# Performance work log

Hardware: AMD Instinct MI355X
Metric: run time of the kernel (lower is better)

The kernel has to match this reference:

```python
import jax, jax.numpy as jnp
import numpy as np

HIDDEN = 2048
HEADS = 16
HEAD_DIM = HIDDEN // HEADS
ROPE_BASE = 10000.0
BSZ, SEQ = 1, 2048
F32_MIN = jnp.finfo(jnp.float32).min


def setup_inputs() -> dict:
    key = jax.random.key(0)
    ks = jax.random.split(key, 5)
    hidden_states = jax.random.normal(ks[0], (BSZ, SEQ, HIDDEN), dtype=jnp.float32)
    # causal additive mask: 0 on/below diagonal, large negative above
    causal = jnp.tril(jnp.ones((SEQ, SEQ), dtype=bool))
    attention_mask = jnp.where(causal, 0.0, F32_MIN)[None, None, :, :].astype(jnp.float32)
    position_ids = jnp.broadcast_to(jnp.arange(SEQ, dtype=jnp.int32)[None, :], (BSZ, SEQ))
    scale = 1.0 / np.sqrt(HIDDEN)
    Wq = jax.random.normal(ks[1], (HIDDEN, HIDDEN), dtype=jnp.float32) * scale
    Wk = jax.random.normal(ks[2], (HIDDEN, HIDDEN), dtype=jnp.float32) * scale
    Wv = jax.random.normal(ks[3], (HIDDEN, HIDDEN), dtype=jnp.float32) * scale
    Wo = jax.random.normal(ks[4], (HIDDEN, HIDDEN), dtype=jnp.float32) * scale
    return {"hidden_states": hidden_states, "attention_mask": attention_mask,
            "position_ids": position_ids, "Wq": Wq, "Wk": Wk, "Wv": Wv, "Wo": Wo}


def _rotate_half(x):
    x1, x2 = jnp.split(x, 2, axis=-1)
    return jnp.concatenate([-x2, x1], axis=-1)


def _rope_cos_sin(position_ids, dtype):
    # [b, s] int -> cos/sin [b, 1, s, head_dim]
    inv_freq = 1.0 / (ROPE_BASE ** (jnp.arange(0, HEAD_DIM, 2, dtype=jnp.float32) / HEAD_DIM))
    freqs = position_ids.astype(jnp.float32)[..., None] * inv_freq  # [b, s, d/2]
    emb = jnp.concatenate([freqs, freqs], axis=-1)  # [b, s, d]
    return jnp.cos(emb)[:, None].astype(dtype), jnp.sin(emb)[:, None].astype(dtype)


def reference(hidden_states, attention_mask, position_ids, Wq, Wk, Wv, Wo):
    b, s, _ = hidden_states.shape

    def proj(W):  # [b, s, hidden] -> [b, h, s, d]
        return jnp.einsum('bsm,mn->bsn', hidden_states, W).reshape(b, s, HEADS, HEAD_DIM).transpose(0, 2, 1, 3)

    q, k, v = proj(Wq), proj(Wk), proj(Wv)
    cos, sin = _rope_cos_sin(position_ids, q.dtype)
    q = q * cos + _rotate_half(q) * sin
    k = k * cos + _rotate_half(k) * sin

    scores = jnp.einsum('bhqd,bhkd->bhqk', q, k) / np.sqrt(HEAD_DIM)
    scores = jnp.maximum(scores + attention_mask, F32_MIN)
    attn = jax.nn.softmax(scores.astype(jnp.float32), axis=-1).astype(q.dtype)
    out = jnp.einsum('bhqk,bhkd->bhqd', attn, v)  # [b, h, s, d]
    out = out.transpose(0, 2, 1, 3).reshape(b, s, HIDDEN)
    return jnp.einsum('bsm,mn->bsn', out, Wo)
```

## Files before the change

kernel.cpp:

```cpp
#include <hip/hip_runtime.h>
#include <hip/hip_bf16.h>
#include <math.h>

#define SEQn 2048
#define HID  2048
#define NH   16
#define HD   128

typedef __attribute__((ext_vector_type(8))) __bf16 bf16x8;
typedef __attribute__((ext_vector_type(4))) float  f32x4;

#define MFMA16(a,b,c) __builtin_amdgcn_mfma_f32_16x16x32_bf16((a),(b),(c),0,0,0)

__device__ __forceinline__ ushort f2bf(float f) {
  union { float f; unsigned u; } v; v.f = f;
  unsigned r = v.u + 0x7fffu + ((v.u >> 16) & 1u);
  return (ushort)(r >> 16);
}
__device__ __forceinline__ float bf2f(ushort u) {
  union { unsigned u; float f; } v; v.u = ((unsigned)u) << 16; return v.f;
}
__device__ __forceinline__ void split2(float x, ushort& h, ushort& l) {
  h = f2bf(x);
  l = f2bf(x - bf2f(h));
}
__device__ __forceinline__ void gl_lds16(const ushort* g, ushort* l) {
  __builtin_amdgcn_global_load_lds((const __attribute__((address_space(1))) unsigned int*)g,
                                   (__attribute__((address_space(3))) unsigned int*)l, 16, 0, 0);
}

__global__ void k_rope_tables(const int* __restrict__ pos,
                              float* __restrict__ cosT, float* __restrict__ sinT) {
  int t = threadIdx.x;
  int s = blockIdx.x * 4 + (t >> 6), i = t & 63;
  float p = (float)pos[s];
  float ex = (float)(2 * i) / 128.0f;
  float invf = 1.0f / powf(10000.0f, ex);
  float f = p * invf;
  cosT[s * 64 + i] = cosf(f);
  sinT[s * 64 + i] = sinf(f);
}

__global__ void k_split(const float* __restrict__ x,
                        ushort* __restrict__ hi, ushort* __restrict__ lo, int n4) {
  int i = blockIdx.x * blockDim.x + threadIdx.x;
  if (i >= n4) return;
  const float4 v = ((const float4*)x)[i];
  ushort4 h, l;
  split2(v.x, h.x, l.x); split2(v.y, h.y, l.y);
  split2(v.z, h.z, l.z); split2(v.w, h.w, l.w);
  ((ushort4*)hi)[i] = h; ((ushort4*)lo)[i] = l;
}

__global__ void k_splitT3(const float* __restrict__ W0, const float* __restrict__ W1,
                          const float* __restrict__ W2,
                          ushort* __restrict__ Th, ushort* __restrict__ Tl) {
  __shared__ float tile[32][33];
  const float* W = (blockIdx.z == 0) ? W0 : (blockIdx.z == 1) ? W1 : W2;
  ushort* Thz = Th + (size_t)blockIdx.z * HID * HID;
  ushort* Tlz = Tl + (size_t)blockIdx.z * HID * HID;
  int kb = blockIdx.x * 32, nb = blockIdx.y * 32;
  int tx = threadIdx.x, ty = threadIdx.y;
#pragma unroll
  for (int r = 0; r < 4; r++)
    tile[ty + r * 8][tx] = W[(size_t)(kb + ty + r * 8) * HID + nb + tx];
  __syncthreads();
#pragma unroll
  for (int r = 0; r < 4; r++) {
    int n = nb + ty + r * 8, k = kb + tx;
    ushort h, l; split2(tile[tx][ty + r * 8], h, l);
    Thz[(size_t)n * HID + k] = h;
    Tlz[(size_t)n * HID + k] = l;
  }
}

template<int DB>
__global__ __launch_bounds__(512) void k_gemm_x3(
    const ushort* __restrict__ Ah, const ushort* __restrict__ Al,
    const ushort* __restrict__ Bh, const ushort* __restrict__ Bl,
    float* __restrict__ C) {
  __shared__ alignas(16) ushort lds[DB][4][4096];
  const int t = threadIdx.x, lane = t & 63, w = t >> 6;
  const int bm = blockIdx.y * 128, bn = blockIdx.x * 128;
  const size_t zb = (size_t)blockIdx.z * HID * HID;
  const int lr = lane & 15, lg = lane >> 4;
  const int sr = t >> 2, sc = (t & 3) * 8;
  const ushort* ga  = Ah + (size_t)(bm + sr) * HID + sc;
  const ushort* gal = Al + (size_t)(bm + sr) * HID + sc;
  const ushort* gb  = Bh + zb + (size_t)(bn + sr) * HID + sc;
  const ushort* gbl = Bl + zb + (size_t)(bn + sr) * HID + sc;
  const int wr = (w & 3) * 32, wc = (w >> 2) * 64;
  f32x4 acc[2][4] = {};
  int cur = 0;
  if constexpr (DB == 2) {
    gl_lds16(ga,  &lds[0][0][w * 512]);
    gl_lds16(gal, &lds[0][1][w * 512]);
    gl_lds16(gb,  &lds[0][2][w * 512]);
    gl_lds16(gbl, &lds[0][3][w * 512]);
  }
  for (int k0 = 0; k0 < HID; k0 += 32) {
    __syncthreads();
    if constexpr (DB == 2) {
      if (k0 + 32 < HID) {
        gl_lds16(ga  + k0 + 32, &lds[cur ^ 1][0][w * 512]);
        gl_lds16(gal + k0 + 32, &lds[cur ^ 1][1][w * 512]);
        gl_lds16(gb  + k0 + 32, &lds[cur ^ 1][2][w * 512]);
        gl_lds16(gbl + k0 + 32, &lds[cur ^ 1][3][w * 512]);
      }
    } else {
      gl_lds16(ga  + k0, &lds[0][0][w * 512]);
      gl_lds16(gal + k0, &lds[0][1][w * 512]);
      gl_lds16(gb  + k0, &lds[0][2][w * 512]);
      gl_lds16(gbl + k0, &lds[0][3][w * 512]);
      __syncthreads();
    }
    bf16x8 a_h[2], a_l[2], b_h[4], b_l[4];
#pragma unroll
    for (int mi = 0; mi < 2; mi++) {
      int ro = (wr + mi * 16 + lr) * 32 + lg * 8;
      a_h[mi] = *(const bf16x8*)&lds[cur][0][ro];
      a_l[mi] = *(const bf16x8*)&lds[cur][1][ro];
    }
#pragma unroll
    for (int ni = 0; ni < 4; ni++) {
      int ro = (wc + ni * 16 + lr) * 32 + lg * 8;
      b_h[ni] = *(const bf16x8*)&lds[cur][2][ro];
      b_l[ni] = *(const bf16x8*)&lds[cur][3][ro];
    }
#pragma unroll
    for (int mi = 0; mi < 2; mi++)
#pragma unroll
      for (int ni = 0; ni < 4; ni++) {
        acc[mi][ni] = MFMA16(a_h[mi], b_h[ni], acc[mi][ni]);
        acc[mi][ni] = MFMA16(a_h[mi], b_l[ni], acc[mi][ni]);
        acc[mi][ni] = MFMA16(a_l[mi], b_h[ni], acc[mi][ni]);
      }
    if constexpr (DB == 2) cur ^= 1;
  }
  float* Cz = C + (size_t)blockIdx.z * SEQn * HID;
#pragma unroll
  for (int mi = 0; mi < 2; mi++)
#pragma unroll
    for (int ni = 0; ni < 4; ni++)
#pragma unroll
      for (int j = 0; j < 4; j++) {
        int row = bm + wr + mi * 16 + lg * 4 + j;
        int col = bn + wc + ni * 16 + lr;
        Cz[(size_t)row * HID + col] = acc[mi][ni][j];
      }
}

__global__ void k_rope_qk(const float* __restrict__ Qf, const float* __restrict__ Kf,
                          const float* __restrict__ cosT, const float* __restrict__ sinT,
                          ushort* __restrict__ Qhh, ushort* __restrict__ Qll,
                          ushort* __restrict__ Khh, ushort* __restrict__ Kll) {
  int t = threadIdx.x;
  int s = blockIdx.x * 4 + (t >> 6), h = blockIdx.y, d = t & 63;
  const float scale = 0.08838834764831845f;
  float c = cosT[s * 64 + d], sn = sinT[s * 64 + d];
  size_t in0  = (size_t)s * HID + h * HD + d;
  size_t out0 = ((size_t)h * SEQn + s) * HD + d;
  ushort hh, ll;
  {
    float q1 = Qf[in0] * scale, q2 = Qf[in0 + 64] * scale;
    split2(q1 * c - q2 * sn, hh, ll); Qhh[out0] = hh;      Qll[out0] = ll;
    split2(q2 * c + q1 * sn, hh, ll); Qhh[out0 + 64] = hh; Qll[out0 + 64] = ll;
  }
  {
    float k1 = Kf[in0], k2 = Kf[in0 + 64];
    split2(k1 * c - k2 * sn, hh, ll); Khh[out0] = hh;      Kll[out0] = ll;
    split2(k2 * c + k1 * sn, hh, ll); Khh[out0 + 64] = hh; Kll[out0 + 64] = ll;
  }
}

__global__ void k_transpose_v(const float* __restrict__ Vf,
                              ushort* __restrict__ Vth, ushort* __restrict__ Vtl) {
  __shared__ float tile[32][33];
  int h = blockIdx.x, db = blockIdx.y * 32, sb = blockIdx.z * 32;
  int tx = threadIdx.x, ty = threadIdx.y;
#pragma unroll
  for (int r = 0; r < 4; r++)
    tile[ty + r * 8][tx] = Vf[(size_t)(sb + ty + r * 8) * HID + h * HD + db + tx];
  __syncthreads();
#pragma unroll
  for (int r = 0; r < 4; r++) {
    int d = db + ty + r * 8, s = sb + tx;
    ushort hh, ll; split2(tile[tx][ty + r * 8], hh, ll);
    size_t o = ((size_t)h * HD + d) * SEQn + s;
    Vth[o] = hh; Vtl[o] = ll;
  }
}

__global__ __launch_bounds__(256) void k_attn(
    const ushort* __restrict__ Qhh, const ushort* __restrict__ Qll,
    const ushort* __restrict__ Khh, const ushort* __restrict__ Kll,
    const ushort* __restrict__ Vth, const ushort* __restrict__ Vtl,
    ushort* __restrict__ Ohi, ushort* __restrict__ Olo) {
  __shared__ alignas(16) ushort sKh[2][8192];
  __shared__ alignas(16) ushort sKl[2][8192];
  __shared__ alignas(16) ushort sVh[2][8192];
  __shared__ alignas(16) ushort sVl[2][8192];
  __shared__ alignas(16) ushort sP[4][1152];
  const int t = threadIdx.x, lane = t & 63, w = t >> 6;
  const int flat = blockIdx.y * 32 + blockIdx.x;
  const int s_ = flat & 255, halfsel = flat >> 8;
  const int qt_ = s_ & 31, h_ = s_ >> 5;
  const int qt = halfsel ? (31 - qt_) : qt_;
  const int h  = halfsel ? (8 + h_) : h_;
  const int qb = qt * 64;
  const int lr = lane & 15, lg = lane >> 4;
  const int q0 = qb + w * 16;
  const size_t qoff = ((size_t)h * SEQn + q0 + lr) * HD + lg * 8;
  bf16x8 qh[4], ql[4];
#pragma unroll
  for (int ks = 0; ks < 4; ks++) {
    qh[ks] = *(const bf16x8*)(Qhh + qoff + ks * 32);
    ql[ks] = *(const bf16x8*)(Qll + qoff + ks * 32);
  }
  const int cc = (w << 6) | lane;
  const int rK = cc >> 4;
  const int cbK = (((cc & 15) << 4) ^ ((rK & 7) << 4)) >> 1;
  const size_t srcKo = (size_t)(h * SEQn + rK) * HD + cbK;
  const int rV = cc >> 3;
  const int cbV = (((cc & 7) << 4) ^ ((rV & 7) << 4)) >> 1;
  const size_t srcVo = (size_t)(h * HD + rV) * SEQn + cbV;

  f32x4 o[8] = {};
  float mrow[4], lrow[4];
#pragma unroll
  for (int j = 0; j < 4; j++) { mrow[j] = -INFINITY; lrow[j] = 0.f; }
  ushort* myp = &sP[w][0];

  {
    const ushort* gKh = Khh + srcKo;
    const ushort* gKl = Kll + srcKo;
    const ushort* gVh = Vth + srcVo;
    const ushort* gVl = Vtl + srcVo;
#pragma unroll
    for (int i = 0; i < 4; i++) {
      gl_lds16(gKh + (size_t)i * 16 * HD,   &sKh[0][(w + i * 4) * 512]);
      gl_lds16(gKl + (size_t)i * 16 * HD,   &sKl[0][(w + i * 4) * 512]);
      gl_lds16(gVh + (size_t)i * 32 * SEQn, &sVh[0][(w + i * 4) * 512]);
      gl_lds16(gVl + (size_t)i * 32 * SEQn, &sVl[0][(w + i * 4) * 512]);
    }
  }

  for (int kv0 = 0; kv0 <= qb; kv0 += 64) {
    const int cur = (kv0 >> 6) & 1;
    __syncthreads();
    if (kv0 + 64 <= qb) {
      const ushort* gKh = Khh + srcKo + (size_t)(kv0 + 64) * HD;
      const ushort* gKl = Kll + srcKo + (size_t)(kv0 + 64) * HD;
      const ushort* gVh = Vth + srcVo + kv0 + 64;
      const ushort* gVl = Vtl + srcVo + kv0 + 64;
#pragma unroll
      for (int i = 0; i < 4; i++) {
        gl_lds16(gKh + (size_t)i * 16 * HD,   &sKh[cur ^ 1][(w + i * 4) * 512]);
        gl_lds16(gKl + (size_t)i * 16 * HD,   &sKl[cur ^ 1][(w + i * 4) * 512]);
        gl_lds16(gVh + (size_t)i * 32 * SEQn, &sVh[cur ^ 1][(w + i * 4) * 512]);
        gl_lds16(gVl + (size_t)i * 32 * SEQn, &sVl[cur ^ 1][(w + i * 4) * 512]);
      }
    }
    f32x4 s4[4] = {};
    __builtin_amdgcn_s_setprio(1);
#pragma unroll
    for (int ni = 0; ni < 4; ni++) {
      const int kr = ni * 16 + lr;
      const int kbase = kr * 128;
      const int ksw = (kr & 7) << 4;
#pragma unroll
      for (int ks = 0; ks < 4; ks++) {
        const int off = kbase + (((ks * 64 + lg * 16) ^ ksw) >> 1);
        bf16x8 kh = *(const bf16x8*)&sKh[cur][off];
        bf16x8 kl = *(const bf16x8*)&sKl[cur][off];
        s4[ni] = MFMA16(qh[ks], kh, s4[ni]);
        s4[ni] = MFMA16(qh[ks], kl, s4[ni]);
        s4[ni] = MFMA16(ql[ks], kh, s4[ni]);
      }
    }
    __builtin_amdgcn_s_setprio(0);
    float sf[4];
    ushort pl[4][4];
#pragma unroll
    for (int j = 0; j < 4; j++) {
      const int row = q0 + lg * 4 + j;
      float sc[4];
#pragma unroll
      for (int ni = 0; ni < 4; ni++) {
        int col = kv0 + ni * 16 + lr;
        sc[ni] = (col <= row) ? s4[ni][j] : -INFINITY;
      }
      float rm = fmaxf(fmaxf(sc[0], sc[1]), fmaxf(sc[2], sc[3]));
#pragma unroll
      for (int off = 1; off < 16; off <<= 1) rm = fmaxf(rm, __shfl_xor(rm, off));
      float mn = fmaxf(mrow[j], rm);
      sf[j] = __expf(mrow[j] - mn);
      float rs = 0.f;
#pragma unroll
      for (int ni = 0; ni < 4; ni++) {
        float pv = __expf(sc[ni] - mn);
        rs += pv;
        ushort hh, ll; split2(pv, hh, ll);
        myp[(lg * 4 + j) * 72 + ni * 16 + lr] = hh;
        pl[j][ni] = ll;
      }
#pragma unroll
      for (int off = 1; off < 16; off <<= 1) rs += __shfl_xor(rs, off);
      lrow[j] = lrow[j] * sf[j] + rs;
      mrow[j] = mn;
    }
#pragma unroll
    for (int nn = 0; nn < 8; nn++) {
      o[nn][0] *= sf[0]; o[nn][1] *= sf[1]; o[nn][2] *= sf[2]; o[nn][3] *= sf[3];
    }
    bf16x8 p0h = *(const bf16x8*)&myp[lr * 72 + lg * 8];
    bf16x8 p1h = *(const bf16x8*)&myp[lr * 72 + lg * 8 + 32];
#pragma unroll
    for (int j = 0; j < 4; j++)
#pragma unroll
      for (int ni = 0; ni < 4; ni++)
        myp[(lg * 4 + j) * 72 + ni * 16 + lr] = pl[j][ni];
    bf16x8 p0l = *(const bf16x8*)&myp[lr * 72 + lg * 8];
    bf16x8 p1l = *(const bf16x8*)&myp[lr * 72 + lg * 8 + 32];
    __builtin_amdgcn_s_setprio(1);
#pragma unroll
    for (int nn = 0; nn < 8; nn++) {
      const int d = nn * 16 + lr;
      const int vbase = d * 64;
      const int vsw = (d & 7) << 4;
      const int o0 = vbase + (((lg * 16) ^ vsw) >> 1);
      const int o1 = vbase + (((lg * 16 + 64) ^ vsw) >> 1);
      bf16x8 vh0 = *(const bf16x8*)&sVh[cur][o0];
      bf16x8 vl0 = *(const bf16x8*)&sVl[cur][o0];
      bf16x8 vh1 = *(const bf16x8*)&sVh[cur][o1];
      bf16x8 vl1 = *(const bf16x8*)&sVl[cur][o1];
      o[nn] = MFMA16(p0h, vh0, o[nn]);
      o[nn] = MFMA16(p0h, vl0, o[nn]);
      o[nn] = MFMA16(p0l, vh0, o[nn]);
      o[nn] = MFMA16(p1h, vh1, o[nn]);
      o[nn] = MFMA16(p1h, vl1, o[nn]);
      o[nn] = MFMA16(p1l, vh1, o[nn]);
    }
    __builtin_amdgcn_s_setprio(0);
  }
#pragma unroll
  for (int nn = 0; nn < 8; nn++)
#pragma unroll
    for (int j = 0; j < 4; j++) {
      int row = q0 + lg * 4 + j;
      int col = h * HD + nn * 16 + lr;
      ushort hh, ll; split2(o[nn][j] / lrow[j], hh, ll);
      Ohi[(size_t)row * HID + col] = hh;
      Olo[(size_t)row * HID + col] = ll;
    }
}

extern "C" void kernel_launch(void* const* d_in, const int* in_sizes, int n_in,
                              void* d_out, int out_size, void* d_ws, size_t ws_size,
                              hipStream_t stream) {
  const float* Hf  = (const float*)d_in[0];
  const int*   pos = (const int*)d_in[2];
  const float* Wq  = (const float*)d_in[3];
  const float* Wk  = (const float*)d_in[4];
  const float* Wv  = (const float*)d_in[5];
  const float* Wo  = (const float*)d_in[6];

  char* ws = (char*)d_ws;
  const size_t SZ_TBL = (size_t)SEQn * 64 * 4;
  const size_t SZ_BF  = (size_t)SEQn * HID * 2;
  const size_t SZ_F   = (size_t)SEQn * HID * 4;
  const size_t PLANE  = (size_t)HID * HID;
  size_t off = 0;
  float*  cosT = (float*)(ws + off);  off += SZ_TBL;
  float*  sinT = (float*)(ws + off);  off += SZ_TBL;
  ushort* Hhi  = (ushort*)(ws + off); off += SZ_BF;
  ushort* Hlo  = (ushort*)(ws + off); off += SZ_BF;
  ushort* W3h  = (ushort*)(ws + off); off += 3 * SZ_BF;
  ushort* W3l  = (ushort*)(ws + off); off += 3 * SZ_BF;
  float*  QKVf = (float*)(ws + off);  off += 3 * SZ_F;
  float*  Qf = QKVf;
  float*  Kf = QKVf + (size_t)SEQn * HID;
  float*  Vf = QKVf + 2 * (size_t)SEQn * HID;
  ushort* Qhh = W3h;
  ushort* Qll = W3h + PLANE;
  ushort* Khh = W3h + 2 * PLANE;
  ushort* Kll = W3l;
  ushort* Vth = W3l + PLANE;
  ushort* Vtl = W3l + 2 * PLANE;
  ushort* Ohi = (ushort*)Kf;
  ushort* Olo = (ushort*)((char*)Kf + SZ_BF);

  const int n4 = SEQn * HID / 4;

  k_rope_tables<<<dim3(SEQn / 4), dim3(256), 0, stream>>>(pos, cosT, sinT);
  k_split<<<dim3(n4 / 256), dim3(256), 0, stream>>>(Hf, Hhi, Hlo, n4);

  k_splitT3<<<dim3(64, 64, 3), dim3(32, 8), 0, stream>>>(Wq, Wk, Wv, W3h, W3l);

  k_gemm_x3<1><<<dim3(16, 16, 3), dim3(512), 0, stream>>>(Hhi, Hlo, W3h, W3l, QKVf);

  k_rope_qk<<<dim3(SEQn / 4, NH), dim3(256), 0, stream>>>(Qf, Kf, cosT, sinT, Qhh, Qll, Khh, Kll);
  k_transpose_v<<<dim3(NH, 4, 64), dim3(32, 8), 0, stream>>>(Vf, Vth, Vtl);

  k_attn<<<dim3(SEQn / 64, NH), dim3(256), 0, stream>>>(Qhh, Qll, Khh, Kll, Vth, Vtl, Ohi, Olo);

  k_splitT3<<<dim3(64, 64, 1), dim3(32, 8), 0, stream>>>(Wo, Wo, Wo, W3h, W3l);
  k_gemm_x3<2><<<dim3(16, 16, 1), dim3(512), 0, stream>>>(Ohi, Olo, W3h, W3l, (float*)d_out);
}
```

Baseline: 585.7 us.

## Drop K/V double buffering and read V directly from global memory

Removes the double-buffered LDS staging for K and V. K is now loaded into a single LDS buffer each iteration, with an extra barrier before use, and the V fragments are read straight from global memory inside the PV loop. This cuts LDS usage from about 137KB to about 41KB, which may allow more resident blocks per CU. In exchange the K load is no longer overlapped with compute, and V is read from global memory by each wave with no sharing through LDS.

```diff
diff --git a/kernel.cpp b/kernel.cpp
--- a/kernel.cpp
+++ b/kernel.cpp
@@ -196,10 +196,8 @@
     const ushort* __restrict__ Khh, const ushort* __restrict__ Kll,
     const ushort* __restrict__ Vth, const ushort* __restrict__ Vtl,
     ushort* __restrict__ Ohi, ushort* __restrict__ Olo) {
-  __shared__ alignas(16) ushort sKh[2][8192];
-  __shared__ alignas(16) ushort sKl[2][8192];
-  __shared__ alignas(16) ushort sVh[2][8192];
-  __shared__ alignas(16) ushort sVl[2][8192];
+  __shared__ alignas(16) ushort sKh[8192];
+  __shared__ alignas(16) ushort sKl[8192];
   __shared__ alignas(16) ushort sP[4][1152];
   const int t = threadIdx.x, lane = t & 63, w = t >> 6;
   const int flat = blockIdx.y * 32 + blockIdx.x;
@@ -221,9 +219,6 @@
   const int rK = cc >> 4;
   const int cbK = (((cc & 15) << 4) ^ ((rK & 7) << 4)) >> 1;
   const size_t srcKo = (size_t)(h * SEQn + rK) * HD + cbK;
-  const int rV = cc >> 3;
-  const int cbV = (((cc & 7) << 4) ^ ((rV & 7) << 4)) >> 1;
-  const size_t srcVo = (size_t)(h * HD + rV) * SEQn + cbV;
 
   f32x4 o[8] = {};
   float mrow[4], lrow[4];
@@ -231,36 +226,18 @@
   for (int j = 0; j < 4; j++) { mrow[j] = -INFINITY; lrow[j] = 0.f; }
   ushort* myp = &sP[w][0];
 
-  {
-    const ushort* gKh = Khh + srcKo;
-    const ushort* gKl = Kll + srcKo;
-    const ushort* gVh = Vth + srcVo;
-    const ushort* gVl = Vtl + srcVo;
-#pragma unroll
-    for (int i = 0; i < 4; i++) {
-      gl_lds16(gKh + (size_t)i * 16 * HD,   &sKh[0][(w + i * 4) * 512]);
-      gl_lds16(gKl + (size_t)i * 16 * HD,   &sKl[0][(w + i * 4) * 512]);
-      gl_lds16(gVh + (size_t)i * 32 * SEQn, &sVh[0][(w + i * 4) * 512]);
-      gl_lds16(gVl + (size_t)i * 32 * SEQn, &sVl[0][(w + i * 4) * 512]);
-    }
-  }
-
   for (int kv0 = 0; kv0 <= qb; kv0 += 64) {
-    const int cur = (kv0 >> 6) & 1;
     __syncthreads();
-    if (kv0 + 64 <= qb) {
-      const ushort* gKh = Khh + srcKo + (size_t)(kv0 + 64) * HD;
-      const ushort* gKl = Kll + srcKo + (size_t)(kv0 + 64) * HD;
-      const ushort* gVh = Vth + srcVo + kv0 + 64;
-      const ushort* gVl = Vtl + srcVo + kv0 + 64;
+    {
+      const ushort* gKh = Khh + srcKo + (size_t)kv0 * HD;
+      const ushort* gKl = Kll + srcKo + (size_t)kv0 * HD;
 #pragma unroll
       for (int i = 0; i < 4; i++) {
-        gl_lds16(gKh + (size_t)i * 16 * HD,   &sKh[cur ^ 1][(w + i * 4) * 512]);
-        gl_lds16(gKl + (size_t)i * 16 * HD,   &sKl[cur ^ 1][(w + i * 4) * 512]);
-        gl_lds16(gVh + (size_t)i * 32 * SEQn, &sVh[cur ^ 1][(w + i * 4) * 512]);
-        gl_lds16(gVl + (size_t)i * 32 * SEQn, &sVl[cur ^ 1][(w + i * 4) * 512]);
-      }
-    }
+        gl_lds16(gKh + (size_t)i * 16 * HD, &sKh[(w + i * 4) * 512]);
+        gl_lds16(gKl + (size_t)i * 16 * HD, &sKl[(w + i * 4) * 512]);
+      }
+    }
+    __syncthreads();
     f32x4 s4[4] = {};
     __builtin_amdgcn_s_setprio(1);
 #pragma unroll
@@ -271,8 +248,8 @@
 #pragma unroll
       for (int ks = 0; ks < 4; ks++) {
         const int off = kbase + (((ks * 64 + lg * 16) ^ ksw) >> 1);
-        bf16x8 kh = *(const bf16x8*)&sKh[cur][off];
-        bf16x8 kl = *(const bf16x8*)&sKl[cur][off];
+        bf16x8 kh = *(const bf16x8*)&sKh[off];
+        bf16x8 kl = *(const bf16x8*)&sKl[off];
         s4[ni] = MFMA16(qh[ks], kh, s4[ni]);
         s4[ni] = MFMA16(qh[ks], kl, s4[ni]);
         s4[ni] = MFMA16(ql[ks], kh, s4[ni]);
@@ -325,15 +302,11 @@
     __builtin_amdgcn_s_setprio(1);
 #pragma unroll
     for (int nn = 0; nn < 8; nn++) {
-      const int d = nn * 16 + lr;
-      const int vbase = d * 64;
-      const int vsw = (d & 7) << 4;
-      const int o0 = vbase + (((lg * 16) ^ vsw) >> 1);
-      const int o1 = vbase + (((lg * 16 + 64) ^ vsw) >> 1);
-      bf16x8 vh0 = *(const bf16x8*)&sVh[cur][o0];
-      bf16x8 vl0 = *(const bf16x8*)&sVl[cur][o0];
-      bf16x8 vh1 = *(const bf16x8*)&sVh[cur][o1];
-      bf16x8 vl1 = *(const bf16x8*)&sVl[cur][o1];
+      const size_t voff = ((size_t)h * HD + nn * 16 + lr) * SEQn + kv0 + lg * 8;
+      bf16x8 vh0 = *(const bf16x8*)(Vth + voff);
+      bf16x8 vl0 = *(const bf16x8*)(Vtl + voff);
+      bf16x8 vh1 = *(const bf16x8*)(Vth + voff + 32);
+      bf16x8 vl1 = *(const bf16x8*)(Vtl + voff + 32);
       o[nn] = MFMA16(p0h, vh0, o[nn]);
       o[nn] = MFMA16(p0h, vl0, o[nn]);
       o[nn] = MFMA16(p0l, vh0, o[nn]);
```

Result: slower. 608.5 us (+3.9%).
